# Kernel optimization log

Measured on AMD Instinct MI355X. Metric: run time of the kernel, lower is better.

## Reference

```python
import jax, jax.numpy as jnp
import numpy as np

B, N, DIM = 4, 2048, 1024
HEADS, DIM_HEAD = 16, 64
INNER = HEADS * DIM_HEAD  # 1024
SCALE = DIM_HEAD ** -0.5


def setup_inputs() -> dict:
    key = jax.random.key(0)
    k_x, k_qkv, k_out, k_b = jax.random.split(key, 4)
    x = jax.random.normal(k_x, (B, N, DIM), dtype=jnp.float32)
    # nn.Linear weights, stored transposed for x @ W convenience
    w_qkv = jax.random.normal(k_qkv, (DIM, 3 * INNER), dtype=jnp.float32) * (DIM ** -0.5)
    w_out = jax.random.normal(k_out, (INNER, DIM), dtype=jnp.float32) * (INNER ** -0.5)
    b_out = jax.random.normal(k_b, (DIM,), dtype=jnp.float32) * 0.01
    return {"x": x, "w_qkv": w_qkv, "w_out": w_out, "b_out": b_out}


def _split_heads(t):
    # 'b n (h d) -> (b h) n d'
    b, n, _ = t.shape
    return t.reshape(b, n, HEADS, DIM_HEAD).transpose(0, 2, 1, 3).reshape(b * HEADS, n, DIM_HEAD)


def reference(x, w_qkv, w_out, b_out):
    b, n, _ = x.shape
    qkv = x @ w_qkv  # [b, n, 3*inner]
    q, k, v = jnp.split(qkv, 3, axis=-1)
    q = q * SCALE
    q, k, v = map(_split_heads, (q, k, v))  # [(b h), n, d]
    sim = jnp.einsum('bid,bjd->bij', q, k)  # [(b h), n, n]
    a = jax.nn.softmax(sim, axis=-1)
    out = jnp.einsum('bij,bjd->bid', a, v)  # [(b h), n, d]
    # '(b h) n d -> b n (h d)'
    out = out.reshape(b, HEADS, n, DIM_HEAD).transpose(0, 2, 1, 3).reshape(b, n, INNER)
    return out @ w_out + b_out  # dropout p=0.0 is identity
```

## Files before the change

### kernel.cpp

```cpp
#include <hip/hip_runtime.h>
#include <stdint.h>


typedef uint16_t u16;
typedef __bf16 bf16x8 __attribute__((ext_vector_type(8)));
typedef float f32x4 __attribute__((ext_vector_type(4)));
typedef unsigned u32x2 __attribute__((ext_vector_type(2)));
typedef unsigned u32x4 __attribute__((ext_vector_type(4)));

#define AS3(p) ((__attribute__((address_space(3))) uint32_t*)(p))
#define AS1(p) ((const __attribute__((address_space(1))) uint32_t*)(p))

__device__ __forceinline__ void gl_lds16(const void* g, void* lds) {
  __builtin_amdgcn_global_load_lds(AS1(g), AS3(lds), 16, 0, 0);
}

__device__ __forceinline__ u16 f2bf(float f) {
  union { __bf16 b; u16 u; } x; x.b = (__bf16)f;
  return x.u;
}

__global__ void cvt_f32_bf16(const float* __restrict__ in, u16* __restrict__ out, long n) {
  long i = ((long)blockIdx.x * 256 + threadIdx.x) * 8;
  if (i >= n) return;
  u16 r[8];
  #pragma unroll
  for (int j = 0; j < 8; ++j) r[j] = f2bf(in[i + j]);
  *(uint4*)(out + i) = *(const uint4*)r;
}

__global__ void transpose_f2b(const float* __restrict__ in, u16* __restrict__ out, int R, int C) {
  __shared__ u16 tile[32][33];
  int tx = threadIdx.x, ty = threadIdx.y;
  int c0 = blockIdx.x * 32, r0 = blockIdx.y * 32;
  #pragma unroll
  for (int i = 0; i < 4; ++i)
    tile[ty + 8 * i][tx] = f2bf(in[(long)(r0 + ty + 8 * i) * C + c0 + tx]);
  __syncthreads();
  #pragma unroll
  for (int i = 0; i < 4; ++i)
    out[(long)(c0 + ty + 8 * i) * R + r0 + tx] = tile[tx][ty + 8 * i];
}

template <bool BIAS, bool OUTF32>
__global__ __launch_bounds__(256) void gemm_bt(const u16* __restrict__ A, const u16* __restrict__ Bt,
                                               const float* __restrict__ bias, void* __restrict__ Cv,
                                               int M, int N, int K, int qcols, float qscale) {
  __shared__ u16 sA[128 * 32];
  __shared__ u16 sB[128 * 32];
  const int tid = threadIdx.x;
  const int w = tid >> 6, l = tid & 63;
  const int l15 = l & 15, lh = l >> 4;
  const int wr = w >> 1, wc = w & 1;
  const long row0 = (long)blockIdx.y * 128, col0 = (long)blockIdx.x * 128;

  const f32x4 fzero = {0.f, 0.f, 0.f, 0.f};
  f32x4 acc[4][4];
  #pragma unroll
  for (int m = 0; m < 4; ++m)
    #pragma unroll
    for (int n = 0; n < 4; ++n) acc[m][n] = fzero;

  for (int kt = 0; kt < K; kt += 32) {
    __syncthreads();
    #pragma unroll
    for (int i = 0; i < 2; ++i) {
      int c = w * 128 + i * 64 + l;
      gl_lds16(A + (row0 + (c >> 2)) * K + kt + (c & 3) * 8,
               (void*)(sA + (w * 128 + i * 64) * 8));
      gl_lds16(Bt + (col0 + (c >> 2)) * K + kt + (c & 3) * 8,
               (void*)(sB + (w * 128 + i * 64) * 8));
    }
    __syncthreads();
    bf16x8 a[4], b[4];
    #pragma unroll
    for (int m = 0; m < 4; ++m)
      a[m] = *(const bf16x8*)&sA[(wr * 64 + m * 16 + l15) * 32 + lh * 8];
    #pragma unroll
    for (int n = 0; n < 4; ++n)
      b[n] = *(const bf16x8*)&sB[(wc * 64 + n * 16 + l15) * 32 + lh * 8];
    #pragma unroll
    for (int m = 0; m < 4; ++m)
      #pragma unroll
      for (int n = 0; n < 4; ++n)
        acc[m][n] = __builtin_amdgcn_mfma_f32_16x16x32_bf16(a[m], b[n], acc[m][n], 0, 0, 0);
  }

  #pragma unroll
  for (int n = 0; n < 4; ++n) {
    long col = col0 + wc * 64 + n * 16 + l15;
    float bv = 0.f;
    if (BIAS) bv = bias[col];
    float scl = (col < qcols) ? qscale : 1.0f;
    #pragma unroll
    for (int m = 0; m < 4; ++m) {
      #pragma unroll
      for (int r = 0; r < 4; ++r) {
        long row = row0 + wr * 64 + m * 16 + lh * 4 + r;
        if (OUTF32) ((float*)Cv)[row * N + col] = acc[m][n][r] + bv;
        else        ((u16*)Cv)[row * N + col] = f2bf(acc[m][n][r] * scl + bv);
      }
    }
  }
}

__global__ __launch_bounds__(256, 4) void attn_k(const u16* __restrict__ qkv, u16* __restrict__ attn) {
  __shared__ u16 smem[16384];
  const int tid = threadIdx.x;
  const int w = tid >> 6, l = tid & 63;
  const int l15 = l & 15, lh = l >> 4;
  const int b = blockIdx.x >> 4, h = blockIdx.x & 15;
  const int qt = blockIdx.y;
  const long rs = 3072;
  const long qrow0 = (long)b * 2048 + qt * 128;
  const u16* Qg    = qkv + qrow0 * rs + h * 64;
  const u16* Kbase = qkv + (long)b * 2048 * rs + 1024 + h * 64;
  const u16* Vbase = qkv + (long)b * 2048 * rs + 2048 + h * 64;

  #pragma unroll
  for (int i = 0; i < 4; ++i) {
    int c = (w * 4 + i) * 64 + l;
    int row = c >> 3;
    int col8 = ((c & 7) ^ (row & 7)) * 8;
    gl_lds16(Qg + (long)row * rs + col8, (void*)(smem + (w * 4 + i) * 512));
  }
  {
    #pragma unroll
    for (int i = 0; i < 2; ++i) {
      int c = (w * 2 + i) * 64 + l;
      int row = c >> 3;
      int col8 = ((c & 7) ^ (row & 7)) * 8;
      gl_lds16(Kbase + (long)row * rs + col8, (void*)(smem + 8192 + (w * 2 + i) * 512));
    }
    int kv0 = (tid & 31) * 2, d0 = (tid >> 5) * 8;
    const u16* Vg = Vbase + (long)kv0 * rs + d0;
    uint4 va = *(const uint4*)Vg;
    uint4 vb = *(const uint4*)(Vg + rs);
    const u16* pa = (const u16*)&va;
    const u16* pb = (const u16*)&vb;
    #pragma unroll
    for (int jj = 0; jj < 8; ++jj) {
      int d = d0 + jj;
      *(uint32_t*)&smem[12288 + d * 64 + (kv0 ^ ((d & 7) << 3))] =
          (uint32_t)pa[jj] | ((uint32_t)pb[jj] << 16);
    }
  }
  __syncthreads();

  bf16x8 aq[2][2];
  #pragma unroll
  for (int m = 0; m < 2; ++m)
    #pragma unroll
    for (int ks = 0; ks < 2; ++ks) {
      int row = w * 32 + m * 16 + l15;
      aq[m][ks] = *(const bf16x8*)&smem[row * 64 + ((ks * 32 + lh * 8) ^ ((row & 7) << 3))];
    }
  __syncthreads();

  const f32x4 fzero = {0.f, 0.f, 0.f, 0.f};
  float lpart[2] = {0.f, 0.f};
  f32x4 acc[2][4];
  #pragma unroll
  for (int m = 0; m < 2; ++m)
    #pragma unroll
    for (int n = 0; n < 4; ++n) acc[m][n] = fzero;

  for (int t = 0; t < 32; ++t) {
    const int kOff  = (t & 1) ? 0    : 8192;
    const int vOff  = (t & 1) ? 4096 : 12288;
    const int kOffN = (t & 1) ? 8192 : 0;
    const int vOffN = (t & 1) ? 12288 : 4096;

    f32x4 s[2][4];
    #pragma unroll
    for (int m = 0; m < 2; ++m)
      #pragma unroll
      for (int n = 0; n < 4; ++n) s[m][n] = fzero;
    #pragma unroll
    for (int ks = 0; ks < 2; ++ks) {
      bf16x8 bk[4];
      #pragma unroll
      for (int n = 0; n < 4; ++n) {
        int row = n * 16 + l15;
        bk[n] = *(const bf16x8*)&smem[kOff + row * 64 + ((ks * 32 + lh * 8) ^ ((row & 7) << 3))];
      }
      __builtin_amdgcn_s_setprio(1);
      #pragma unroll
      for (int m = 0; m < 2; ++m)
        #pragma unroll
        for (int n = 0; n < 4; ++n)
          s[m][n] = __builtin_amdgcn_mfma_f32_16x16x32_bf16(bk[n], aq[m][ks], s[m][n], 0, 0, 0);
      __builtin_amdgcn_s_setprio(0);
    }

    uint4 kreg[2], va, vb;
    int kv0 = (tid & 31) * 2, d0v = (tid >> 5) * 8;
    if (t < 31) {
      #pragma unroll
      for (int i = 0; i < 2; ++i) {
        int c = (w * 2 + i) * 64 + l;
        int row = c >> 3, sub = c & 7;
        kreg[i] = *(const uint4*)(Kbase + ((long)(t + 1) * 64 + row) * rs + sub * 8);
      }
      const u16* Vg = Vbase + ((long)(t + 1) * 64 + kv0) * rs + d0v;
      va = *(const uint4*)Vg;
      vb = *(const uint4*)(Vg + rs);
    }

    unsigned Wm[2][4][2];
    #pragma unroll
    for (int m = 0; m < 2; ++m) {
      #pragma unroll
      for (int n = 0; n < 4; ++n) {
        float p0 = __builtin_amdgcn_exp2f(s[m][n][0]);
        float p1 = __builtin_amdgcn_exp2f(s[m][n][1]);
        float p2 = __builtin_amdgcn_exp2f(s[m][n][2]);
        float p3 = __builtin_amdgcn_exp2f(s[m][n][3]);
        lpart[m] += (p0 + p1) + (p2 + p3);
        Wm[m][n][0] = (unsigned)f2bf(p0) | ((unsigned)f2bf(p1) << 16);
        Wm[m][n][1] = (unsigned)f2bf(p2) | ((unsigned)f2bf(p3) << 16);
      }
    }

    #pragma unroll
    for (int ks = 0; ks < 2; ++ks) {
      bf16x8 pf[2];
      #pragma unroll
      for (int m = 0; m < 2; ++m) {
        unsigned a0 = Wm[m][2 * ks][0], b0 = Wm[m][2 * ks + 1][0];
        unsigned a1 = Wm[m][2 * ks][1], b1 = Wm[m][2 * ks + 1][1];
        asm("v_permlane32_swap_b32 %0, %1" : "+v"(a0), "+v"(b0));
        asm("v_permlane16_swap_b32 %0, %1" : "+v"(a0), "+v"(b0));
        asm("v_permlane32_swap_b32 %0, %1" : "+v"(a1), "+v"(b1));
        asm("v_permlane16_swap_b32 %0, %1" : "+v"(a1), "+v"(b1));
        union { u32x4 u; bf16x8 f; } cv;
        cv.u = (u32x4){a0, a1, b0, b1};
        pf[m] = cv.f;
      }
      bf16x8 bv4[4];
      #pragma unroll
      for (int n = 0; n < 4; ++n) {
        int vr = n * 16 + l15;
        bv4[n] = *(const bf16x8*)&smem[vOff + vr * 64 + ((ks * 32 + lh * 8) ^ ((vr & 7) << 3))];
      }
      __builtin_amdgcn_s_setprio(1);
      #pragma unroll
      for (int n = 0; n < 4; ++n)
        #pragma unroll
        for (int m = 0; m < 2; ++m)
          acc[m][n] = __builtin_amdgcn_mfma_f32_16x16x32_bf16(bv4[n], pf[m], acc[m][n], 0, 0, 0);
      __builtin_amdgcn_s_setprio(0);
    }

    if (t < 31) {
      #pragma unroll
      for (int i = 0; i < 2; ++i) {
        int c = (w * 2 + i) * 64 + l;
        int row = c >> 3, sub = c & 7;
        *(uint4*)&smem[kOffN + row * 64 + (sub ^ (row & 7)) * 8] = kreg[i];
      }
      const u16* pa = (const u16*)&va;
      const u16* pb = (const u16*)&vb;
      #pragma unroll
      for (int jj = 0; jj < 8; ++jj) {
        int d = d0v + jj;
        *(uint32_t*)&smem[vOffN + d * 64 + (kv0 ^ ((d & 7) << 3))] =
            (uint32_t)pa[jj] | ((uint32_t)pb[jj] << 16);
      }
      __syncthreads();
    }
  }

  #pragma unroll
  for (int m = 0; m < 2; ++m) {
    float lsum = lpart[m];
    lsum += __shfl_xor(lsum, 16);
    lsum += __shfl_xor(lsum, 32);
    float inv = 1.0f / lsum;
    long q = qrow0 + w * 32 + m * 16 + l15;
    #pragma unroll
    for (int n = 0; n < 4; ++n) {
      unsigned lo = (unsigned)f2bf(acc[m][n][0] * inv) | ((unsigned)f2bf(acc[m][n][1] * inv) << 16);
      unsigned hi = (unsigned)f2bf(acc[m][n][2] * inv) | ((unsigned)f2bf(acc[m][n][3] * inv) << 16);
      *(u32x2*)&attn[q * 1024 + h * 64 + n * 16 + lh * 4] = (u32x2){lo, hi};
    }
  }
}

extern "C" void kernel_launch(void* const* d_in, const int* in_sizes, int n_in,
                              void* d_out, int out_size, void* d_ws, size_t ws_size,
                              hipStream_t stream) {
  (void)in_sizes; (void)n_in; (void)out_size; (void)ws_size;
  const float* x     = (const float*)d_in[0];
  const float* w_qkv = (const float*)d_in[1];
  const float* w_out = (const float*)d_in[2];
  const float* b_out = (const float*)d_in[3];
  float* out = (float*)d_out;

  u16* ws    = (u16*)d_ws;
  u16* wqkvT = ws;
  u16* woutT = wqkvT + (size_t)3072 * 1024;
  u16* xbf   = woutT + (size_t)1024 * 1024;
  u16* qkv   = xbf   + (size_t)8192 * 1024;
  u16* attnb = qkv   + (size_t)8192 * 3072;

  const float QSCALE = 0.125f * 1.44269504088896f;

  cvt_f32_bf16<<<4096, 256, 0, stream>>>(x, xbf, (long)8192 * 1024);
  transpose_f2b<<<dim3(96, 32), dim3(32, 8), 0, stream>>>(w_qkv, wqkvT, 1024, 3072);
  transpose_f2b<<<dim3(32, 32), dim3(32, 8), 0, stream>>>(w_out, woutT, 1024, 1024);
  gemm_bt<false, false><<<dim3(24, 64), 256, 0, stream>>>(xbf, wqkvT, nullptr, qkv,
                                                          8192, 3072, 1024, 1024, QSCALE);
  attn_k<<<dim3(64, 16), 256, 0, stream>>>(qkv, attnb);
  gemm_bt<true, true><<<dim3(8, 64), 256, 0, stream>>>(attnb, woutT, b_out, out,
                                                       8192, 1024, 1024, 0, 1.0f);
}
```

Before: 211.3 us.

## Double attention q-tile to 256 rows with 512 threads and MFMA row sums

```diff
diff --git a/kernel.cpp b/kernel.cpp
--- a/kernel.cpp
+++ b/kernel.cpp
@@ -104,15 +104,15 @@
   }
 }
 
-__global__ __launch_bounds__(256, 4) void attn_k(const u16* __restrict__ qkv, u16* __restrict__ attn) {
-  __shared__ u16 smem[16384];
+__global__ __launch_bounds__(512, 4) void attn_k(const u16* __restrict__ qkv, u16* __restrict__ attn) {
+  __shared__ u16 smem[24576];
   const int tid = threadIdx.x;
   const int w = tid >> 6, l = tid & 63;
   const int l15 = l & 15, lh = l >> 4;
   const int b = blockIdx.x >> 4, h = blockIdx.x & 15;
   const int qt = blockIdx.y;
   const long rs = 3072;
-  const long qrow0 = (long)b * 2048 + qt * 128;
+  const long qrow0 = (long)b * 2048 + qt * 256;
   const u16* Qg    = qkv + qrow0 * rs + h * 64;
   const u16* Kbase = qkv + (long)b * 2048 * rs + 1024 + h * 64;
   const u16* Vbase = qkv + (long)b * 2048 * rs + 2048 + h * 64;
@@ -125,23 +125,21 @@
     gl_lds16(Qg + (long)row * rs + col8, (void*)(smem + (w * 4 + i) * 512));
   }
   {
-    #pragma unroll
-    for (int i = 0; i < 2; ++i) {
-      int c = (w * 2 + i) * 64 + l;
-      int row = c >> 3;
-      int col8 = ((c & 7) ^ (row & 7)) * 8;
-      gl_lds16(Kbase + (long)row * rs + col8, (void*)(smem + 8192 + (w * 2 + i) * 512));
-    }
-    int kv0 = (tid & 31) * 2, d0 = (tid >> 5) * 8;
+    int c = tid;
+    int row = c >> 3;
+    int col8 = ((c & 7) ^ (row & 7)) * 8;
+    gl_lds16(Kbase + (long)row * rs + col8, (void*)(smem + 16384 + w * 512));
+
+    int kv0 = (tid & 31) * 2, d0 = (tid >> 5) * 4;
     const u16* Vg = Vbase + (long)kv0 * rs + d0;
-    uint4 va = *(const uint4*)Vg;
-    uint4 vb = *(const uint4*)(Vg + rs);
+    u32x2 va = *(const u32x2*)Vg;
+    u32x2 vb = *(const u32x2*)(Vg + rs);
     const u16* pa = (const u16*)&va;
     const u16* pb = (const u16*)&vb;
     #pragma unroll
-    for (int jj = 0; jj < 8; ++jj) {
+    for (int jj = 0; jj < 4; ++jj) {
       int d = d0 + jj;
-      *(uint32_t*)&smem[12288 + d * 64 + (kv0 ^ ((d & 7) << 3))] =
+      *(uint32_t*)&smem[20480 + d * 64 + (kv0 ^ ((d & 7) << 3))] =
           (uint32_t)pa[jj] | ((uint32_t)pb[jj] << 16);
     }
   }
@@ -157,19 +155,24 @@
     }
   __syncthreads();
 
+  bf16x8 ones;
+  { union { u32x4 u; bf16x8 f; } cv; cv.u = (u32x4){0x3F803F80u, 0x3F803F80u, 0x3F803F80u, 0x3F803F80u}; ones = cv.f; }
+
   const f32x4 fzero = {0.f, 0.f, 0.f, 0.f};
-  float lpart[2] = {0.f, 0.f};
   f32x4 acc[2][4];
-  #pragma unroll
-  for (int m = 0; m < 2; ++m)
+  f32x4 acc_l[2];
+  #pragma unroll
+  for (int m = 0; m < 2; ++m) {
+    acc_l[m] = fzero;
     #pragma unroll
     for (int n = 0; n < 4; ++n) acc[m][n] = fzero;
+  }
 
   for (int t = 0; t < 32; ++t) {
-    const int kOff  = (t & 1) ? 0    : 8192;
-    const int vOff  = (t & 1) ? 4096 : 12288;
-    const int kOffN = (t & 1) ? 8192 : 0;
-    const int vOffN = (t & 1) ? 12288 : 4096;
+    const int kOff  = (t & 1) ? 0     : 16384;
+    const int vOff  = (t & 1) ? 4096  : 20480;
+    const int kOffN = (t & 1) ? 16384 : 0;
+    const int vOffN = (t & 1) ? 20480 : 4096;
 
     f32x4 s[2][4];
     #pragma unroll
@@ -193,18 +196,15 @@
       __builtin_amdgcn_s_setprio(0);
     }
 
-    uint4 kreg[2], va, vb;
-    int kv0 = (tid & 31) * 2, d0v = (tid >> 5) * 8;
+    uint4 kreg;
+    u32x2 va, vb;
+    int kv0 = (tid & 31) * 2, d0v = (tid >> 5) * 4;
     if (t < 31) {
-      #pragma unroll
-      for (int i = 0; i < 2; ++i) {
-        int c = (w * 2 + i) * 64 + l;
-        int row = c >> 3, sub = c & 7;
-        kreg[i] = *(const uint4*)(Kbase + ((long)(t + 1) * 64 + row) * rs + sub * 8);
-      }
+      int row = tid >> 3, sub = tid & 7;
+      kreg = *(const uint4*)(Kbase + ((long)(t + 1) * 64 + row) * rs + sub * 8);
       const u16* Vg = Vbase + ((long)(t + 1) * 64 + kv0) * rs + d0v;
-      va = *(const uint4*)Vg;
-      vb = *(const uint4*)(Vg + rs);
+      va = *(const u32x2*)Vg;
+      vb = *(const u32x2*)(Vg + rs);
     }
 
     unsigned Wm[2][4][2];
@@ -216,7 +216,6 @@
         float p1 = __builtin_amdgcn_exp2f(s[m][n][1]);
         float p2 = __builtin_amdgcn_exp2f(s[m][n][2]);
         float p3 = __builtin_amdgcn_exp2f(s[m][n][3]);
-        lpart[m] += (p0 + p1) + (p2 + p3);
         Wm[m][n][0] = (unsigned)f2bf(p0) | ((unsigned)f2bf(p1) << 16);
         Wm[m][n][1] = (unsigned)f2bf(p2) | ((unsigned)f2bf(p3) << 16);
       }
@@ -249,20 +248,19 @@
         #pragma unroll
         for (int m = 0; m < 2; ++m)
           acc[m][n] = __builtin_amdgcn_mfma_f32_16x16x32_bf16(bv4[n], pf[m], acc[m][n], 0, 0, 0);
+      #pragma unroll
+      for (int m = 0; m < 2; ++m)
+        acc_l[m] = __builtin_amdgcn_mfma_f32_16x16x32_bf16(ones, pf[m], acc_l[m], 0, 0, 0);
       __builtin_amdgcn_s_setprio(0);
     }
 
     if (t < 31) {
-      #pragma unroll
-      for (int i = 0; i < 2; ++i) {
-        int c = (w * 2 + i) * 64 + l;
-        int row = c >> 3, sub = c & 7;
-        *(uint4*)&smem[kOffN + row * 64 + (sub ^ (row & 7)) * 8] = kreg[i];
-      }
+      int row = tid >> 3, sub = tid & 7;
+      *(uint4*)&smem[kOffN + row * 64 + (sub ^ (row & 7)) * 8] = kreg;
       const u16* pa = (const u16*)&va;
       const u16* pb = (const u16*)&vb;
       #pragma unroll
-      for (int jj = 0; jj < 8; ++jj) {
+      for (int jj = 0; jj < 4; ++jj) {
         int d = d0v + jj;
         *(uint32_t*)&smem[vOffN + d * 64 + (kv0 ^ ((d & 7) << 3))] =
             (uint32_t)pa[jj] | ((uint32_t)pb[jj] << 16);
@@ -273,10 +271,7 @@
 
   #pragma unroll
   for (int m = 0; m < 2; ++m) {
-    float lsum = lpart[m];
-    lsum += __shfl_xor(lsum, 16);
-    lsum += __shfl_xor(lsum, 32);
-    float inv = 1.0f / lsum;
+    float inv = 1.0f / acc_l[m][0];
     long q = qrow0 + w * 32 + m * 16 + l15;
     #pragma unroll
     for (int n = 0; n < 4; ++n) {
@@ -311,7 +306,7 @@
   transpose_f2b<<<dim3(32, 32), dim3(32, 8), 0, stream>>>(w_out, woutT, 1024, 1024);
   gemm_bt<false, false><<<dim3(24, 64), 256, 0, stream>>>(xbf, wqkvT, nullptr, qkv,
                                                           8192, 3072, 1024, 1024, QSCALE);
-  attn_k<<<dim3(64, 16), 256, 0, stream>>>(qkv, attnb);
+  attn_k<<<dim3(64, 8), 512, 0, stream>>>(qkv, attnb);
   gemm_bt<true, true><<<dim3(8, 64), 256, 0, stream>>>(attnb, woutT, b_out, out,
                                                        8192, 1024, 1024, 0, 1.0f);
 }
```

Result: faster. 197.1 us (-6.7%).
